# Kernel optimization log

Hardware: AMD Instinct MI355X
Metric: run time of the kernel (lower is better)

## Reference

```python
import jax, jax.numpy as jnp
import numpy as np
from jax import lax

HEADS = 8
DIM_HEAD = 64
LANDMARKS = 256
PINV_ITERS = 6
KERNEL = 33


def moore_penrose_iter_pinv(x, iters=PINV_ITERS):
    # x: [b, h, m, m]
    abs_x = jnp.abs(x)
    col = abs_x.sum(axis=-1)
    row = abs_x.sum(axis=-2)
    z = jnp.swapaxes(x, -1, -2) / (jnp.max(col) * jnp.max(row) + 1e-12)
    I = jnp.eye(x.shape[-1], dtype=x.dtype)  # broadcasts over b, h
    for _ in range(iters):
        xz = x @ z
        z = 0.25 * z @ (13.0 * I - xz @ (15.0 * I - xz @ (7.0 * I - xz)))
    return z


def setup_inputs() -> dict:
    key = jax.random.key(0)
    k1, k2, k3, k4, k5 = jax.random.split(key, 5)
    b, n, dim = 4, 8192, 512
    inner = HEADS * DIM_HEAD
    x = jax.random.normal(k1, (b, n, dim), dtype=jnp.float32)
    Wqkv = jax.random.normal(k2, (dim, inner * 3), dtype=jnp.float32) * (dim ** -0.5)
    Wout = jax.random.normal(k3, (inner, dim), dtype=jnp.float32) * (inner ** -0.5)
    bout = jax.random.normal(k4, (dim,), dtype=jnp.float32) * 0.02
    conv_w = jax.random.normal(k5, (HEADS, 1, KERNEL, 1), dtype=jnp.float32) * (KERNEL ** -0.5)
    return {"x": x, "Wqkv": Wqkv, "Wout": Wout, "bout": bout, "conv_w": conv_w}


def reference(x, Wqkv, Wout, bout, conv_w):
    b, n, dim = x.shape
    h, d, m = HEADS, DIM_HEAD, LANDMARKS
    scale = d ** -0.5
    # n is a multiple of m, so no left-padding branch; mask is None.
    qkv = x @ Wqkv  # [b, n, 3*h*d]
    q, k, v = jnp.split(qkv, 3, axis=-1)
    tohead = lambda t: t.reshape(b, n, h, d).transpose(0, 2, 1, 3)  # [b,h,n,d]
    q, k, v = tohead(q), tohead(k), tohead(v)
    q = q * scale
    l = n // m  # tokens per landmark group
    qL = q.reshape(b, h, m, l, d).sum(axis=3) / l  # [b,h,m,d]
    kL = k.reshape(b, h, m, l, d).sum(axis=3) / l
    attn1 = jax.nn.softmax(jnp.einsum('bhid,bhjd->bhij', q, kL), axis=-1)   # [b,h,n,m]
    attn2 = jax.nn.softmax(jnp.einsum('bhid,bhjd->bhij', qL, kL), axis=-1)  # [b,h,m,m]
    attn3 = jax.nn.softmax(jnp.einsum('bhid,bhjd->bhij', qL, k), axis=-1)   # [b,h,m,n]
    attn2_pinv = moore_penrose_iter_pinv(attn2, PINV_ITERS)
    out = attn1 @ (attn2_pinv @ (attn3 @ v))  # [b,h,n,d]
    # depthwise residual conv over v viewed as NCHW (C=heads, H=n, W=d)
    pad = KERNEL // 2
    res = lax.conv_general_dilated(
        v, conv_w, window_strides=(1, 1), padding=((pad, pad), (0, 0)),
        dimension_numbers=('NCHW', 'OIHW', 'NCHW'), feature_group_count=h)
    out = out + res
    out = out.transpose(0, 2, 1, 3).reshape(b, n, h * d)
    out = out @ Wout + bout
    return out
```

## Files before the change

### kernel.cpp

```cpp
#include <hip/hip_runtime.h>
#include <hip/hip_bf16.h>
#include <math.h>

#define BB 4
#define NH 8
#define NN 8192
#define DD 64
#define MM 256
#define LG 32
#define DIM 512
#define K3 1536
#define KER 33

typedef __hip_bfloat16 bf16;
typedef __attribute__((ext_vector_type(8))) short bf16x8;
typedef __attribute__((ext_vector_type(4))) float f32x4;

__device__ __forceinline__ float b2f(bf16 x) { return __bfloat162float(x); }
__device__ __forceinline__ bf16 f2b(float x) { return __float2bfloat16(x); }
__device__ __forceinline__ short f2bs(float x) { bf16 h = __float2bfloat16(x); return *reinterpret_cast<short*>(&h); }
__device__ __forceinline__ float bsf(short s) { return __uint_as_float(((unsigned int)(unsigned short)s) << 16); }
__device__ __forceinline__ float blo(unsigned int u) { return __uint_as_float(u << 16); }
__device__ __forceinline__ float bhi(unsigned int u) { return __uint_as_float(u & 0xffff0000u); }

__device__ __forceinline__ void g2lds16(const void* g, void* l) {
    __builtin_amdgcn_global_load_lds(
        (const __attribute__((address_space(1))) unsigned int*)g,
        (__attribute__((address_space(3))) unsigned int*)l, 16, 0, 0);
}

__global__ void zero_out(float* __restrict__ o) {
    o[(size_t)blockIdx.x * 256 + threadIdx.x] = 0.f;
}

__global__ void split_x(const float* __restrict__ x, short* __restrict__ xh,
                        short* __restrict__ xl) {
    size_t i = ((size_t)blockIdx.x * 256 + threadIdx.x) * 8;
    const float4* xp = (const float4*)(x + i);
    float4 v0 = xp[0], v1 = xp[1];
    float vv[8] = {v0.x, v0.y, v0.z, v0.w, v1.x, v1.y, v1.z, v1.w};
    short hb[8], lb[8];
#pragma unroll
    for (int u = 0; u < 8; u++) {
        bf16 h = f2b(vv[u]);
        hb[u] = *(short*)&h;
        lb[u] = f2bs(vv[u] - b2f(h));
    }
    *(uint4*)(xh + i) = *(uint4*)hb;
    *(uint4*)(xl + i) = *(uint4*)lb;
}

__global__ void split_wT(const float* __restrict__ W, short* __restrict__ wh,
                         short* __restrict__ wl, int Nn) {
    int idx = blockIdx.x * 256 + threadIdx.x;
    int k = idx & 511, n = idx >> 9;
    float v = W[(size_t)k * Nn + n];
    bf16 h = f2b(v);
    wh[idx] = *(short*)&h;
    wl[idx] = f2bs(v - b2f(h));
}

__global__ __launch_bounds__(256) void gemm_qkv_mfma(
        const short* __restrict__ xh, const short* __restrict__ xl,
        const short* __restrict__ wh, const short* __restrict__ wl,
        bf16* __restrict__ q, bf16* __restrict__ k, bf16* __restrict__ v) {
    __shared__ short Ah[128 * 32];
    __shared__ short Al[128 * 32];
    __shared__ short Bh[128 * 32];
    __shared__ short Bl[128 * 32];
    int orig = blockIdx.x;
    int wg = (orig & 7) * 384 + (orig >> 3);
    int by = wg / 12, bx = wg - by * 12;
    int rowBase = by * 128, colBase = bx * 128;
    int tid = threadIdx.x;
    int rl = tid >> 2;
    int ch = (tid & 3) * 8;
    int wave = tid >> 6, lane = tid & 63;
    int ln = lane & 15, quad = lane >> 4;
    int wr = (wave >> 1) * 64, wc = (wave & 1) * 64;
    f32x4 acc[4][4];
#pragma unroll
    for (int mt = 0; mt < 4; mt++)
#pragma unroll
        for (int nt = 0; nt < 4; nt++) acc[mt][nt] = (f32x4){0.f, 0.f, 0.f, 0.f};

    for (int k0 = 0; k0 < DIM; k0 += 32) {
        __syncthreads();
#pragma unroll
        for (int p = 0; p < 2; p++) {
            int r = p * 64 + rl;
            size_t ga = (size_t)(rowBase + r) * DIM + k0 + ch;
            size_t gb = (size_t)(colBase + r) * DIM + k0 + ch;
            int lo = r * 32 + ch;
            g2lds16(xh + ga, &Ah[lo]);
            g2lds16(xl + ga, &Al[lo]);
            g2lds16(wh + gb, &Bh[lo]);
            g2lds16(wl + gb, &Bl[lo]);
        }
        __syncthreads();
        bf16x8 a_h[4], a_l[4], b_h[4], b_l[4];
#pragma unroll
        for (int mt = 0; mt < 4; mt++) {
            int o = (wr + mt * 16 + ln) * 32 + quad * 8;
            a_h[mt] = *(const bf16x8*)&Ah[o];
            a_l[mt] = *(const bf16x8*)&Al[o];
        }
#pragma unroll
        for (int nt = 0; nt < 4; nt++) {
            int o = (wc + nt * 16 + ln) * 32 + quad * 8;
            b_h[nt] = *(const bf16x8*)&Bh[o];
            b_l[nt] = *(const bf16x8*)&Bl[o];
        }
#pragma unroll
        for (int mt = 0; mt < 4; mt++)
#pragma unroll
            for (int nt = 0; nt < 4; nt++) {
                acc[mt][nt] = __builtin_amdgcn_mfma_f32_16x16x32_bf16(a_h[mt], b_h[nt], acc[mt][nt], 0, 0, 0);
                acc[mt][nt] = __builtin_amdgcn_mfma_f32_16x16x32_bf16(a_l[mt], b_h[nt], acc[mt][nt], 0, 0, 0);
                acc[mt][nt] = __builtin_amdgcn_mfma_f32_16x16x32_bf16(a_h[mt], b_l[nt], acc[mt][nt], 0, 0, 0);
            }
    }
    int part = colBase >> 9;
    bf16* dst = part == 0 ? q : (part == 1 ? k : v);
    float scale = part == 0 ? 0.125f : 1.0f;
#pragma unroll
    for (int mt = 0; mt < 4; mt++)
#pragma unroll
        for (int nt = 0; nt < 4; nt++)
#pragma unroll
            for (int r = 0; r < 4; r++) {
                int row = rowBase + wr + mt * 16 + quad * 4 + r;
                int col = colBase + wc + nt * 16 + ln;
                int h = (col & 511) >> 6, d = col & 63;
                int b_ = row >> 13, n_ = row & 8191;
                size_t di = ((size_t)(b_ * NH + h) * NN + n_) * DD + d;
                dst[di] = f2b(acc[mt][nt][r] * scale);
            }
}

__global__ __launch_bounds__(256) void gemm_out_mfma(
        const bf16* __restrict__ A, const short* __restrict__ wh,
        const short* __restrict__ wl, const float* __restrict__ bias,
        float* __restrict__ C) {
    __shared__ short As[128 * 32];
    __shared__ short Bh[128 * 32];
    __shared__ short Bl[128 * 32];
    int orig = blockIdx.x;
    int wg = (orig & 7) * 128 + (orig >> 3);
    int by = wg >> 2, bx = wg & 3;
    int rowBase = by * 128, colBase = bx * 128;
    int tid = threadIdx.x;
    int rl = tid >> 2, ch = (tid & 3) * 8;
    int wave = tid >> 6, lane = tid & 63;
    int ln = lane & 15, quad = lane >> 4;
    int wr = (wave >> 1) * 64, wc = (wave & 1) * 64;
    const short* Ab = (const short*)A;
    f32x4 acc[4][4];
#pragma unroll
    for (int mt = 0; mt < 4; mt++)
#pragma unroll
        for (int nt = 0; nt < 4; nt++) acc[mt][nt] = (f32x4){0.f, 0.f, 0.f, 0.f};

    for (int k0 = 0; k0 < DIM; k0 += 32) {
        __syncthreads();
#pragma unroll
        for (int p = 0; p < 2; p++) {
            int r = p * 64 + rl;
            size_t ga = (size_t)(rowBase + r) * DIM + k0 + ch;
            size_t gb = (size_t)(colBase + r) * DIM + k0 + ch;
            int lo = r * 32 + ch;
            g2lds16(Ab + ga, &As[lo]);
            g2lds16(wh + gb, &Bh[lo]);
            g2lds16(wl + gb, &Bl[lo]);
        }
        __syncthreads();
        bf16x8 a[4], b_h[4], b_l[4];
#pragma unroll
        for (int mt = 0; mt < 4; mt++)
            a[mt] = *(const bf16x8*)&As[(wr + mt * 16 + ln) * 32 + quad * 8];
#pragma unroll
        for (int nt = 0; nt < 4; nt++) {
            int o = (wc + nt * 16 + ln) * 32 + quad * 8;
            b_h[nt] = *(const bf16x8*)&Bh[o];
            b_l[nt] = *(const bf16x8*)&Bl[o];
        }
#pragma unroll
        for (int mt = 0; mt < 4; mt++)
#pragma unroll
            for (int nt = 0; nt < 4; nt++) {
                acc[mt][nt] = __builtin_amdgcn_mfma_f32_16x16x32_bf16(a[mt], b_h[nt], acc[mt][nt], 0, 0, 0);
                acc[mt][nt] = __builtin_amdgcn_mfma_f32_16x16x32_bf16(a[mt], b_l[nt], acc[mt][nt], 0, 0, 0);
            }
    }
#pragma unroll
    for (int mt = 0; mt < 4; mt++)
#pragma unroll
        for (int nt = 0; nt < 4; nt++)
#pragma unroll
            for (int r = 0; r < 4; r++) {
                int row = rowBase + wr + mt * 16 + quad * 4 + r;
                int col = colBase + wc + nt * 16 + ln;
                C[(size_t)row * DIM + col] = acc[mt][nt][r] + bias[col];
            }
}

__global__ __launch_bounds__(256) void bgemm_pair(
        const short* __restrict__ Ah, const short* __restrict__ Al,
        const short* __restrict__ Bh, const short* __restrict__ Bl,
        short* __restrict__ oAh, short* __restrict__ oAl,
        short* __restrict__ oBh, short* __restrict__ oBl,
        float* __restrict__ oF, float scale, float alpha,
        float scaleB, float alphaB, int flags) {
    __shared__ short sAh[64 * 32];
    __shared__ short sAl[64 * 32];
    __shared__ short sBh[64 * 32];
    __shared__ short sBl[64 * 32];
    int bat = blockIdx.z;
    int rowBase = blockIdx.y * 64;
    int colBase = blockIdx.x * 64;
    const size_t MB = (size_t)bat * (MM * MM);
    int tid = threadIdx.x;
    int rl = tid >> 2, ch = (tid & 3) * 8;
    int wave = tid >> 6, lane = tid & 63;
    int ln = lane & 15, quad = lane >> 4;
    int wr = (wave >> 1) * 32, wc = (wave & 1) * 32;
    f32x4 acc[2][2];
#pragma unroll
    for (int mt = 0; mt < 2; mt++)
#pragma unroll
        for (int nt = 0; nt < 2; nt++) acc[mt][nt] = (f32x4){0.f, 0.f, 0.f, 0.f};

    for (int k0 = 0; k0 < MM; k0 += 32) {
        __syncthreads();
        {
            size_t ga = MB + (size_t)(rowBase + rl) * MM + k0 + ch;
            size_t gb = MB + (size_t)(colBase + rl) * MM + k0 + ch;
            int lo = rl * 32 + ch;
            g2lds16(Ah + ga, &sAh[lo]);
            g2lds16(Al + ga, &sAl[lo]);
            g2lds16(Bh + gb, &sBh[lo]);
            g2lds16(Bl + gb, &sBl[lo]);
        }
        __syncthreads();
        bf16x8 a_h[2], a_l[2], b_h[2], b_l[2];
#pragma unroll
        for (int mt = 0; mt < 2; mt++) {
            int o = (wr + mt * 16 + ln) * 32 + quad * 8;
            a_h[mt] = *(const bf16x8*)&sAh[o];
            a_l[mt] = *(const bf16x8*)&sAl[o];
        }
#pragma unroll
        for (int nt = 0; nt < 2; nt++) {
            int o = (wc + nt * 16 + ln) * 32 + quad * 8;
            b_h[nt] = *(const bf16x8*)&sBh[o];
            b_l[nt] = *(const bf16x8*)&sBl[o];
        }
#pragma unroll
        for (int mt = 0; mt < 2; mt++)
#pragma unroll
            for (int nt = 0; nt < 2; nt++) {
                acc[mt][nt] = __builtin_amdgcn_mfma_f32_16x16x32_bf16(a_h[mt], b_h[nt], acc[mt][nt], 0, 0, 0);
                acc[mt][nt] = __builtin_amdgcn_mfma_f32_16x16x32_bf16(a_l[mt], b_h[nt], acc[mt][nt], 0, 0, 0);
                acc[mt][nt] = __builtin_amdgcn_mfma_f32_16x16x32_bf16(a_h[mt], b_l[nt], acc[mt][nt], 0, 0, 0);
            }
    }
#pragma unroll
    for (int mt = 0; mt < 2; mt++)
#pragma unroll
        for (int nt = 0; nt < 2; nt++) {
            short bh4[4], bl4[4];
            int col = colBase + wc + nt * 16 + ln;
            int row0 = rowBase + wr + mt * 16 + quad * 4;
#pragma unroll
            for (int r = 0; r < 4; r++) {
                int row = row0 + r;
                float val = scale * acc[mt][nt][r];
                if (row == col) val += alpha;
                if (flags & 4) oF[MB + (size_t)row * MM + col] = val;
                if (flags & 1) {
                    short vh = f2bs(val);
                    oAh[MB + (size_t)row * MM + col] = vh;
                    oAl[MB + (size_t)row * MM + col] = f2bs(val - bsf(vh));
                }
                float bv = scaleB * val;
                if (row == col) bv += alphaB;
                short bvh = f2bs(bv);
                bh4[r] = bvh; bl4[r] = f2bs(bv - bsf(bvh));
            }
            if (flags & 2) {
                size_t o = MB + (size_t)col * MM + row0;
                *(uint2*)&oBh[o] = *(uint2*)bh4;
                *(uint2*)&oBl[o] = *(uint2*)bl4;
            }
        }
}

__global__ void z_init_split(const float* __restrict__ x2, const float* __restrict__ scal,
                             short* __restrict__ x2Ah, short* __restrict__ x2Al,
                             short* __restrict__ zAh, short* __restrict__ zAl,
                             short* __restrict__ zBh, short* __restrict__ zBl) {
    size_t base = ((size_t)blockIdx.x * 256 + threadIdx.x) * 8;
    float inv = 1.0f / (scal[0] + 1e-12f);
    int c0 = (int)(base & 255);
    int r = (int)((base >> 8) & 255);
    size_t MB = (base >> 16) << 16;
    const float4* xp = (const float4*)(x2 + base);
    float4 v0 = xp[0], v1 = xp[1];
    float vv[8] = {v0.x, v0.y, v0.z, v0.w, v1.x, v1.y, v1.z, v1.w};
    short ho[8], lo_[8], h2[8], l2[8];
#pragma unroll
    for (int u = 0; u < 8; u++) {
        short xh = f2bs(vv[u]);
        h2[u] = xh; l2[u] = f2bs(vv[u] - bsf(xh));
        float zv = vv[u] * inv;
        short zh = f2bs(zv);
        ho[u] = zh; lo_[u] = f2bs(zv - bsf(zh));
    }
    *(uint4*)&x2Ah[base] = *(uint4*)h2;
    *(uint4*)&x2Al[base] = *(uint4*)l2;
    *(uint4*)&zBh[base] = *(uint4*)ho;
    *(uint4*)&zBl[base] = *(uint4*)lo_;
#pragma unroll
    for (int u = 0; u < 8; u++) {
        float v = x2[MB + (size_t)(c0 + u) * MM + r] * inv;
        short vh = f2bs(v);
        ho[u] = vh; lo_[u] = f2bs(v - bsf(vh));
    }
    *(uint4*)&zAh[base] = *(uint4*)ho;
    *(uint4*)&zAl[base] = *(uint4*)lo_;
}

__global__ void bgemm_t2t(const float* __restrict__ A, const float* __restrict__ B,
                          short* __restrict__ T) {
    __shared__ float As[16][64];
    __shared__ float Bs[16][64];
    int bat = blockIdx.z;
    const float* Ab = A + (size_t)bat * MM * MM;
    const float* Bb = B + (size_t)bat * MM * DD;
    short* Tb = T + (size_t)bat * DD * MM;
    int tid = threadIdx.x;
    int rowBase = blockIdx.y * 64;
    int ty = tid >> 4, tx = tid & 15;
    float acc[4][4] = {};
    for (int k0 = 0; k0 < MM; k0 += 16) {
        for (int idx = tid; idx < 64 * 16; idx += 256) {
            int r = idx >> 4, c = idx & 15;
            As[c][r] = Ab[(size_t)(rowBase + r) * MM + k0 + c];
        }
        for (int idx = tid; idx < 16 * 64; idx += 256) {
            int r = idx >> 6, c = idx & 63;
            Bs[r][c] = Bb[(size_t)(k0 + r) * DD + c];
        }
        __syncthreads();
#pragma unroll
        for (int kk = 0; kk < 16; kk++) {
            float a[4], b[4];
#pragma unroll
            for (int i = 0; i < 4; i++) a[i] = As[kk][ty * 4 + i];
#pragma unroll
            for (int j = 0; j < 4; j++) b[j] = Bs[kk][tx * 4 + j];
#pragma unroll
            for (int i = 0; i < 4; i++)
#pragma unroll
                for (int j = 0; j < 4; j++) acc[i][j] += a[i] * b[j];
        }
        __syncthreads();
    }
#pragma unroll
    for (int i = 0; i < 4; i++) {
        int r = rowBase + ty * 4 + i;
#pragma unroll
        for (int j = 0; j < 4; j++) {
            int c = tx * 4 + j;
            Tb[(size_t)c * MM + r] = f2bs(acc[i][j]);
        }
    }
}

__global__ void landmark_means(const bf16* __restrict__ q, const bf16* __restrict__ k,
                               float* __restrict__ qL, float* __restrict__ kL) {
    int idx = blockIdx.x * 256 + threadIdx.x;
    int d = idx & 63;
    int mi = (idx >> 6) & 255;
    int bh = idx >> 14;
    const bf16* qp = q + ((size_t)bh * NN + mi * LG) * DD + d;
    const bf16* kp = k + ((size_t)bh * NN + mi * LG) * DD + d;
    float sq = 0.f, sk = 0.f;
#pragma unroll
    for (int j = 0; j < LG; j++) { sq += b2f(qp[(size_t)j * DD]); sk += b2f(kp[(size_t)j * DD]); }
    qL[idx] = sq * (1.f / LG);
    kL[idx] = sk * (1.f / LG);
}

__global__ void kl_to_bf16(const float* __restrict__ kL, short* __restrict__ kl16) {
    size_t i = ((size_t)blockIdx.x * 256 + threadIdx.x) * 4;
    float4 v = *(const float4*)(kL + i);
    short o[4] = {f2bs(v.x), f2bs(v.y), f2bs(v.z), f2bs(v.w)};
    *(uint2*)&kl16[i] = *(uint2*)o;
}

__global__ void attn2_softmax(const float* __restrict__ qL, const float* __restrict__ kL,
                              float* __restrict__ x2) {
    __shared__ float qs[64];
    __shared__ float red[256];
    int bh = blockIdx.x >> 8, i = blockIdx.x & 255;
    int t = threadIdx.x;
    if (t < 64) qs[t] = qL[((size_t)bh * MM + i) * DD + t];
    __syncthreads();
    const float4* kp = (const float4*)(kL + ((size_t)bh * MM + t) * DD);
    float l = 0.f;
#pragma unroll
    for (int u = 0; u < 16; u++) {
        float4 kv = kp[u];
        l += qs[u*4+0]*kv.x + qs[u*4+1]*kv.y + qs[u*4+2]*kv.z + qs[u*4+3]*kv.w;
    }
    red[t] = l; __syncthreads();
    for (int s = 128; s > 0; s >>= 1) { if (t < s) red[t] = fmaxf(red[t], red[t + s]); __syncthreads(); }
    float mx = red[0]; __syncthreads();
    float e = __expf(l - mx);
    red[t] = e; __syncthreads();
    for (int s = 128; s > 0; s >>= 1) { if (t < s) red[t] += red[t + s]; __syncthreads(); }
    x2[((size_t)bh * MM + i) * MM + t] = e / red[0];
}

__global__ void init_scal(float* scal) {
    if (threadIdx.x == 0) { scal[0] = 0.f; scal[1] = 0.f; }
}

__global__ void csum_max(const float* __restrict__ x2, float* scal) {
    __shared__ float red[256];
    int t = threadIdx.x;
    const float* xp = x2 + (size_t)blockIdx.x * MM * MM;
    float s = 0.f;
    for (int i = 0; i < MM; i++) s += fabsf(xp[(size_t)i * MM + t]);
    red[t] = s; __syncthreads();
    for (int st = 128; st > 0; st >>= 1) { if (t < st) red[t] = fmaxf(red[t], red[t + st]); __syncthreads(); }
    if (t == 0) atomicMax((unsigned int*)&scal[0], __float_as_uint(red[0]));
}

__global__ void transpose_v(const bf16* __restrict__ v, bf16* __restrict__ vT) {
    int gw = blockIdx.x * 4 + (threadIdx.x >> 6);
    int lane = threadIdx.x & 63;
    int bh = gw >> 8;
    int c  = gw & 255;
    const bf16* vb = v + ((size_t)bh * NN + c * 32) * DD + lane;
    unsigned short buf[32];
#pragma unroll
    for (int i = 0; i < 32; i++) buf[i] = *(const unsigned short*)(vb + (size_t)i * DD);
    bf16* dst = vT + ((size_t)bh * DD + lane) * NN + c * 32;
#pragma unroll
    for (int u = 0; u < 4; u++)
        *(uint4*)(dst + u * 8) = *(uint4*)&buf[u * 8];
}

#define NJ 128
#define KS2 72
#define VS2 136
#define PS2 136
__global__ __launch_bounds__(128, 2) void attn3v_mfma(
        const float* __restrict__ qL, const bf16* __restrict__ k,
        const bf16* __restrict__ vT, float* __restrict__ t1) {
    __shared__ short ks[NJ * KS2];
    __shared__ short vs[DD * VS2];
    __shared__ short ps[2][16 * PS2];
    int g = blockIdx.x;
    int c = g & 7, t = g >> 3;
    int bh = c + 8 * (t >> 3);
    int r0 = (t & 7) * 32;
    int tid = threadIdx.x;
    int wave = tid >> 6, lane = tid & 63;
    int ln = lane & 15, quad = lane >> 4;
    int m = r0 + wave * 16 + ln;
    const float* qrow = qL + ((size_t)bh * MM + m) * DD;
    bf16x8 a0, a1;
#pragma unroll
    for (int u = 0; u < 8; u++) {
        ((short*)&a0)[u] = f2bs(qrow[quad * 8 + u]);
        ((short*)&a1)[u] = f2bs(qrow[32 + quad * 8 + u]);
    }
    const uint4* kg = (const uint4*)(k + (size_t)bh * NN * DD);
    const uint4* vg = (const uint4*)(vT + (size_t)bh * DD * NN);
    float mrow[4], lrow[4];
    f32x4 o[4];
#pragma unroll
    for (int r = 0; r < 4; r++) { mrow[r] = -1e30f; lrow[r] = 0.f; }
#pragma unroll
    for (int ct = 0; ct < 4; ct++) o[ct] = (f32x4){0.f, 0.f, 0.f, 0.f};
    short* pw = &ps[wave][0];

    for (int j0 = 0; j0 < NN; j0 += NJ) {
        __syncthreads();
#pragma unroll
        for (int it = 0; it < 8; it++) {
            int idx = it * 128 + tid;
            int row = idx >> 3, c8 = idx & 7;
            uint4 pk = kg[(size_t)(j0 + row) * 8 + c8];
            *(uint4*)&ks[row * KS2 + c8 * 8] = pk;
        }
#pragma unroll
        for (int it = 0; it < 8; it++) {
            int idx = it * 128 + tid;
            int row = idx >> 4, c8 = idx & 15;
            uint4 pv = vg[(size_t)row * (NN / 8) + (j0 / 8) + c8];
            *(uint4*)&vs[row * VS2 + c8 * 8] = pv;
        }
        __syncthreads();
        f32x4 s[8];
#pragma unroll
        for (int ct = 0; ct < 8; ct++) {
            const short* kp = &ks[(ct * 16 + ln) * KS2 + quad * 8];
            bf16x8 b0 = *(const bf16x8*)kp;
            bf16x8 b1 = *(const bf16x8*)(kp + 32);
            f32x4 cc = {0.f, 0.f, 0.f, 0.f};
            cc = __builtin_amdgcn_mfma_f32_16x16x32_bf16(a0, b0, cc, 0, 0, 0);
            cc = __builtin_amdgcn_mfma_f32_16x16x32_bf16(a1, b1, cc, 0, 0, 0);
            s[ct] = cc;
        }
#pragma unroll
        for (int r = 0; r < 4; r++) {
            float v = -1e30f;
#pragma unroll
            for (int ct = 0; ct < 8; ct++) v = fmaxf(v, s[ct][r]);
            v = fmaxf(v, __shfl_xor(v, 1));
            v = fmaxf(v, __shfl_xor(v, 2));
            v = fmaxf(v, __shfl_xor(v, 4));
            v = fmaxf(v, __shfl_xor(v, 8));
            float mn = fmaxf(mrow[r], v);
            float alpha = __expf(mrow[r] - mn);
            mrow[r] = mn;
            float psum = 0.f;
#pragma unroll
            for (int ct = 0; ct < 8; ct++) { float e = __expf(s[ct][r] - mn); s[ct][r] = e; psum += e; }
            lrow[r] = lrow[r] * alpha + psum;
#pragma unroll
            for (int c2 = 0; c2 < 4; c2++) o[c2][r] *= alpha;
        }
#pragma unroll
        for (int ct = 0; ct < 8; ct++)
#pragma unroll
            for (int r = 0; r < 4; r++)
                pw[(quad * 4 + r) * PS2 + ct * 16 + ln] = f2bs(s[ct][r]);
#pragma unroll
        for (int kstep = 0; kstep < 4; kstep++) {
            bf16x8 pa = *(const bf16x8*)&pw[ln * PS2 + kstep * 32 + quad * 8];
#pragma unroll
            for (int ct = 0; ct < 4; ct++) {
                bf16x8 pb = *(const bf16x8*)&vs[(ct * 16 + ln) * VS2 + kstep * 32 + quad * 8];
                o[ct] = __builtin_amdgcn_mfma_f32_16x16x32_bf16(pa, pb, o[ct], 0, 0, 0);
            }
        }
    }
#pragma unroll
    for (int r = 0; r < 4; r++) {
        float l = lrow[r];
        l += __shfl_xor(l, 1);
        l += __shfl_xor(l, 2);
        l += __shfl_xor(l, 4);
        l += __shfl_xor(l, 8);
        lrow[r] = 1.0f / l;
    }
#pragma unroll
    for (int ct = 0; ct < 4; ct++)
#pragma unroll
        for (int r = 0; r < 4; r++) {
            int row = r0 + wave * 16 + quad * 4 + r;
            t1[((size_t)bh * MM + row) * DD + ct * 16 + ln] = o[ct][r] * lrow[r];
        }
}

#define T2S 264
#define VLS 72
__global__ __launch_bounds__(256, 3) void attn1_mfma(
        const bf16* __restrict__ q, const short* __restrict__ kl16,
        const short* __restrict__ t2t, const bf16* __restrict__ v,
        const float* __restrict__ cw, bf16* __restrict__ oh) {
    __shared__ short ps1[4][16 * T2S];
    __shared__ short vload[96 * VLS];
    int bh = blockIdx.y;
    int n0 = blockIdx.x * 64;
    int tid = threadIdx.x;
    int b_ = bh >> 3, h = bh & 7;
    const bf16* vb = v + (size_t)bh * NN * DD;
    for (int idx = tid; idx < 96 * 8; idx += 256) {
        int row = idx >> 3, c8 = (idx & 7) * 8;
        int gn = n0 - 16 + row;
        uint4 pv;
        pv.x = pv.y = pv.z = pv.w = 0u;
        if (gn >= 0 && gn < NN) pv = *(const uint4*)(vb + (size_t)gn * DD + c8);
        *(uint4*)&vload[row * VLS + c8] = pv;
    }
    int wave = tid >> 6, lane = tid & 63;
    int ln = lane & 15, quad = lane >> 4;
    int m = n0 + wave * 16 + ln;
    const bf16* qrow = q + ((size_t)bh * NN + m) * DD;
    bf16x8 a0 = *(const bf16x8*)(qrow + quad * 8);
    bf16x8 a1 = *(const bf16x8*)(qrow + 32 + quad * 8);
    const short* klb = kl16 + (size_t)bh * MM * DD;
    f32x4 acc[16];
#pragma unroll
    for (int nt = 0; nt < 16; nt++) {
        const short* kp = klb + (nt * 16 + ln) * DD + quad * 8;
        bf16x8 b0 = *(const bf16x8*)kp;
        bf16x8 b1 = *(const bf16x8*)(kp + 32);
        f32x4 c = {0.f, 0.f, 0.f, 0.f};
        c = __builtin_amdgcn_mfma_f32_16x16x32_bf16(a0, b0, c, 0, 0, 0);
        c = __builtin_amdgcn_mfma_f32_16x16x32_bf16(a1, b1, c, 0, 0, 0);
        acc[nt] = c;
    }
    float inv[4];
#pragma unroll
    for (int r = 0; r < 4; r++) {
        float vx = -1e30f;
#pragma unroll
        for (int nt = 0; nt < 16; nt++) vx = fmaxf(vx, acc[nt][r]);
        vx = fmaxf(vx, __shfl_xor(vx, 1));
        vx = fmaxf(vx, __shfl_xor(vx, 2));
        vx = fmaxf(vx, __shfl_xor(vx, 4));
        vx = fmaxf(vx, __shfl_xor(vx, 8));
        float s = 0.f;
#pragma unroll
        for (int nt = 0; nt < 16; nt++) { float e = __expf(acc[nt][r] - vx); acc[nt][r] = e; s += e; }
        s += __shfl_xor(s, 1);
        s += __shfl_xor(s, 2);
        s += __shfl_xor(s, 4);
        s += __shfl_xor(s, 8);
        inv[r] = 1.0f / s;
    }
    short* pw = &ps1[wave][0];
#pragma unroll
    for (int nt = 0; nt < 16; nt++)
#pragma unroll
        for (int r = 0; r < 4; r++)
            pw[(quad * 4 + r) * T2S + nt * 16 + ln] = f2bs(acc[nt][r]);
    __syncthreads();
    const short* t2b = t2t + (size_t)bh * DD * MM;
    f32x4 o[4];
#pragma unroll
    for (int nt = 0; nt < 4; nt++) o[nt] = (f32x4){0.f, 0.f, 0.f, 0.f};
#pragma unroll
    for (int ks = 0; ks < 8; ks++) {
        bf16x8 pa = *(const bf16x8*)&pw[ln * T2S + ks * 32 + quad * 8];
#pragma unroll
        for (int nt = 0; nt < 4; nt++) {
            bf16x8 pb = *(const bf16x8*)(t2b + (nt * 16 + ln) * MM + ks * 32 + quad * 8);
            o[nt] = __builtin_amdgcn_mfma_f32_16x16x32_bf16(pa, pb, o[nt], 0, 0, 0);
        }
    }
    const float* wrow = cw + h * KER;
    int lbase = wave * 16 + quad * 4;
#pragma unroll
    for (int nt = 0; nt < 4; nt++) {
        int d = nt * 16 + ln;
        float win[36];
#pragma unroll
        for (int j = 0; j < 36; j++)
            win[j] = bsf(vload[(lbase + j) * VLS + d]);
        float res[4] = {0.f, 0.f, 0.f, 0.f};
#pragma unroll
        for (int t = 0; t < KER; t++) {
            float wt = wrow[t];
#pragma unroll
            for (int r = 0; r < 4; r++) res[r] += wt * win[r + t];
        }
#pragma unroll
        for (int r = 0; r < 4; r++) {
            int row = n0 + lbase + r;
            oh[((size_t)(b_ * NN + row)) * DIM + h * 64 + d] = f2b(o[nt][r] * inv[r] + res[r]);
        }
    }
}


extern "C" void kernel_launch(void* const* d_in, const int* in_sizes, int n_in,
                              void* d_out, int out_size, void* d_ws, size_t ws_size,
                              hipStream_t stream) {
    const float* x    = (const float*)d_in[0];
    const float* Wqkv = (const float*)d_in[1];
    const float* Wout = (const float*)d_in[2];
    const float* bout = (const float*)d_in[3];
    const float* cw   = (const float*)d_in[4];
    float* out = (float*)d_out;

    const size_t SZ_QKV = (size_t)BB * NH * NN * DD;
    const size_t SZ_L   = (size_t)BB * NH * MM * DD;
    const size_t SZ_M2  = (size_t)BB * NH * MM * MM;

    char* p = (char*)d_ws;
    bf16* q    = (bf16*)p;  p += SZ_QKV * 2;
    bf16* v    = (bf16*)p;  p += SZ_QKV * 2;
    float* x2   = (float*)p; p += SZ_M2 * 4;
    float* zf   = (float*)p; p += SZ_M2 * 4;
    float* z2r  = (float*)p; p += SZ_M2 * 4;
    float* bAr  = (float*)p; p += SZ_M2 * 4;
    float* bBr  = (float*)p; p += SZ_M2 * 4;
    float* qL   = (float*)p; p += SZ_L * 4;
    float* kL   = (float*)p; p += SZ_L * 4;
    float* t1   = (float*)p; p += SZ_L * 4;
    short* t2t  = (short*)p; p += SZ_L * 4;
    float* scal = (float*)p; p += 2 * 4;
    size_t need = (size_t)(p - (char*)d_ws);
    bf16* k  = (bf16*)d_out;
    bf16* vT = (bf16*)d_out + SZ_QKV;
    bf16* oh = (bf16*)x2;

    short* xh  = (short*)x2;
    short* xl  = (short*)vT;
    short* wqh = (short*)bBr;
    short* wql = (short*)bBr + (size_t)K3 * DIM;
    short* woh = (short*)q;
    short* wol = (short*)q + (size_t)DIM * DIM;
    short* kl16 = (short*)t1;

    const size_t U = SZ_M2;
    short* db = (short*)d_out;
    short* bufBTh = db + 0 * U;  short* bufBTl = db + 1 * U;
    short* z2BTh  = db + 2 * U;  short* z2BTl  = db + 3 * U;
    short* zPair[2][4] = {
        { db + 4 * U, db + 5 * U, db + 6 * U, db + 7 * U },
        { db + 8 * U, db + 9 * U, db + 10 * U, db + 11 * U } };
    short* x2Ah = (short*)z2r;   short* x2Al = (short*)z2r + U;
    short* bufAh = (short*)bAr;  short* bufAl = (short*)bAr + U;

    if (ws_size < need) {
        zero_out<<<out_size / 256, 256, 0, stream>>>(out);
        return;
    }

    split_x<<<(int)(SZ_QKV / (256 * 8)), 256, 0, stream>>>(x, xh, xl);
    split_wT<<<(K3 * DIM) / 256, 256, 0, stream>>>(Wqkv, wqh, wql, K3);
    gemm_qkv_mfma<<<3072, 256, 0, stream>>>(xh, xl, wqh, wql, q, k, v);
    transpose_v<<<(BB * NH * MM) / 4, 256, 0, stream>>>(v, vT);
    landmark_means<<<(BB * NH * MM * DD) / 256, 256, 0, stream>>>(q, k, qL, kL);
    attn2_softmax<<<BB * NH * MM, 256, 0, stream>>>(qL, kL, x2);
    attn3v_mfma<<<256, 128, 0, stream>>>(qL, k, vT, t1);
    init_scal<<<1, 64, 0, stream>>>(scal);
    csum_max<<<BB * NH, 256, 0, stream>>>(x2, scal);
    z_init_split<<<(int)(SZ_M2 / (256 * 8)), 256, 0, stream>>>(
        x2, scal, x2Ah, x2Al,
        zPair[0][0], zPair[0][1], zPair[0][2], zPair[0][3]);
    int cur = 0;
    for (int it = 0; it < 6; it++) {
        int nxt = cur ^ 1;
        bgemm_pair<<<dim3(4, 4, BB * NH), 256, 0, stream>>>(
            x2Ah, x2Al, zPair[cur][2], zPair[cur][3],
            bufAh, bufAl, bufBTh, bufBTl, nullptr,
            1.f, 0.f, -1.f, 7.f, 1 | 2);
        bgemm_pair<<<dim3(4, 4, BB * NH), 256, 0, stream>>>(
            bufAh, bufAl, bufBTh, bufBTl,
            nullptr, nullptr, z2BTh, z2BTl, nullptr,
            -1.f, 15.f, 1.f, 0.f, 2);
        bgemm_pair<<<dim3(4, 4, BB * NH), 256, 0, stream>>>(
            bufAh, bufAl, z2BTh, z2BTl,
            nullptr, nullptr, bufBTh, bufBTl, nullptr,
            -1.f, 13.f, 1.f, 0.f, 2);
        int fl = (it == 5) ? 4 : (1 | 2);
        bgemm_pair<<<dim3(4, 4, BB * NH), 256, 0, stream>>>(
            zPair[cur][0], zPair[cur][1], bufBTh, bufBTl,
            zPair[nxt][0], zPair[nxt][1], zPair[nxt][2], zPair[nxt][3],
            zf, 0.25f, 0.f, 1.f, 0.f, fl);
        cur = nxt;
    }
    bgemm_t2t<<<dim3(1, 4, BB * NH), 256, 0, stream>>>(zf, t1, t2t);
    kl_to_bf16<<<(int)(SZ_L / (256 * 4)), 256, 0, stream>>>(kL, kl16);
    attn1_mfma<<<dim3(NN / 64, BB * NH), 256, 0, stream>>>(q, kl16, t2t, v, cw, oh);
    split_wT<<<(DIM * DIM) / 256, 256, 0, stream>>>(Wout, woh, wol, DIM);
    gemm_out_mfma<<<1024, 256, 0, stream>>>(oh, woh, wol, bout, out);

    (void)in_sizes; (void)n_in; (void)ws_size;
}
```

Baseline: 1.044 ms.

## Split attn3v key range across wave pairs and transpose conv window in LDS

The attn3v kernel now runs 256 threads per block. Two wave pairs each process alternating 128-key chunks with their own K/V shared buffers, and their online-softmax states (max, sum, output) are merged through shared memory at the end. This doubles parallelism over the sequential 8192-key loop, since only 256 blocks were launched, at the cost of more LDS and a merge step. Separately, attn1 stores the v window transposed in LDS so each lane reads its 36-tap conv window with 8-byte vector loads instead of strided scalar reads.

```diff
diff --git a/kernel.cpp b/kernel.cpp
--- a/kernel.cpp
+++ b/kernel.cpp
@@ -457,20 +457,23 @@
 #define KS2 72
 #define VS2 136
 #define PS2 136
-__global__ __launch_bounds__(128, 2) void attn3v_mfma(
+__global__ __launch_bounds__(256) void attn3v_mfma(
         const float* __restrict__ qL, const bf16* __restrict__ k,
         const bf16* __restrict__ vT, float* __restrict__ t1) {
-    __shared__ short ks[NJ * KS2];
-    __shared__ short vs[DD * VS2];
-    __shared__ short ps[2][16 * PS2];
+    __shared__ short ks[2][NJ * KS2];
+    __shared__ short vs[2][DD * VS2];
+    __shared__ short ps[4][16 * PS2];
+    __shared__ float mb[128 * 25];
     int g = blockIdx.x;
     int c = g & 7, t = g >> 3;
     int bh = c + 8 * (t >> 3);
     int r0 = (t & 7) * 32;
     int tid = threadIdx.x;
     int wave = tid >> 6, lane = tid & 63;
+    int pair = wave >> 1, wv = wave & 1;
+    int ptid = tid & 127;
     int ln = lane & 15, quad = lane >> 4;
-    int m = r0 + wave * 16 + ln;
+    int m = r0 + wv * 16 + ln;
     const float* qrow = qL + ((size_t)bh * MM + m) * DD;
     bf16x8 a0, a1;
 #pragma unroll
@@ -487,28 +490,31 @@
 #pragma unroll
     for (int ct = 0; ct < 4; ct++) o[ct] = (f32x4){0.f, 0.f, 0.f, 0.f};
     short* pw = &ps[wave][0];
-
-    for (int j0 = 0; j0 < NN; j0 += NJ) {
-        __syncthreads();
-#pragma unroll
-        for (int it = 0; it < 8; it++) {
-            int idx = it * 128 + tid;
+    short* ksp = &ks[pair][0];
+    short* vsp = &vs[pair][0];
+
+    for (int it = 0; it < NN / (2 * NJ); it++) {
+        int j0 = (2 * it + pair) * NJ;
+        __syncthreads();
+#pragma unroll
+        for (int s = 0; s < 8; s++) {
+            int idx = s * 128 + ptid;
             int row = idx >> 3, c8 = idx & 7;
             uint4 pk = kg[(size_t)(j0 + row) * 8 + c8];
-            *(uint4*)&ks[row * KS2 + c8 * 8] = pk;
-        }
-#pragma unroll
-        for (int it = 0; it < 8; it++) {
-            int idx = it * 128 + tid;
+            *(uint4*)&ksp[row * KS2 + c8 * 8] = pk;
+        }
+#pragma unroll
+        for (int s = 0; s < 8; s++) {
+            int idx = s * 128 + ptid;
             int row = idx >> 4, c8 = idx & 15;
             uint4 pv = vg[(size_t)row * (NN / 8) + (j0 / 8) + c8];
-            *(uint4*)&vs[row * VS2 + c8 * 8] = pv;
+            *(uint4*)&vsp[row * VS2 + c8 * 8] = pv;
         }
         __syncthreads();
         f32x4 s[8];
 #pragma unroll
         for (int ct = 0; ct < 8; ct++) {
-            const short* kp = &ks[(ct * 16 + ln) * KS2 + quad * 8];
+            const short* kp = &ksp[(ct * 16 + ln) * KS2 + quad * 8];
             bf16x8 b0 = *(const bf16x8*)kp;
             bf16x8 b1 = *(const bf16x8*)(kp + 32);
             f32x4 cc = {0.f, 0.f, 0.f, 0.f};
@@ -545,37 +551,62 @@
             bf16x8 pa = *(const bf16x8*)&pw[ln * PS2 + kstep * 32 + quad * 8];
 #pragma unroll
             for (int ct = 0; ct < 4; ct++) {
-                bf16x8 pb = *(const bf16x8*)&vs[(ct * 16 + ln) * VS2 + kstep * 32 + quad * 8];
+                bf16x8 pb = *(const bf16x8*)&vsp[(ct * 16 + ln) * VS2 + kstep * 32 + quad * 8];
                 o[ct] = __builtin_amdgcn_mfma_f32_16x16x32_bf16(pa, pb, o[ct], 0, 0, 0);
             }
         }
     }
-#pragma unroll
-    for (int r = 0; r < 4; r++) {
-        float l = lrow[r];
-        l += __shfl_xor(l, 1);
-        l += __shfl_xor(l, 2);
-        l += __shfl_xor(l, 4);
-        l += __shfl_xor(l, 8);
-        lrow[r] = 1.0f / l;
-    }
-#pragma unroll
-    for (int ct = 0; ct < 4; ct++)
+    __syncthreads();
+    if (wave >= 2) {
+        float* mp = &mb[(tid - 128) * 25];
+#pragma unroll
+        for (int r = 0; r < 4; r++) { mp[r] = mrow[r]; mp[4 + r] = lrow[r]; }
+#pragma unroll
+        for (int ct = 0; ct < 4; ct++)
+#pragma unroll
+            for (int r = 0; r < 4; r++) mp[8 + ct * 4 + r] = o[ct][r];
+    }
+    __syncthreads();
+    if (wave < 2) {
+        const float* mp = &mb[(wave * 64 + lane) * 25];
 #pragma unroll
         for (int r = 0; r < 4; r++) {
-            int row = r0 + wave * 16 + quad * 4 + r;
-            t1[((size_t)bh * MM + row) * DD + ct * 16 + ln] = o[ct][r] * lrow[r];
-        }
+            float mB = mp[r], lB = mp[4 + r];
+            float mn = fmaxf(mrow[r], mB);
+            float eA = __expf(mrow[r] - mn);
+            float eB = __expf(mB - mn);
+            lrow[r] = lrow[r] * eA + lB * eB;
+#pragma unroll
+            for (int ct = 0; ct < 4; ct++)
+                o[ct][r] = o[ct][r] * eA + mp[8 + ct * 4 + r] * eB;
+        }
+#pragma unroll
+        for (int r = 0; r < 4; r++) {
+            float l = lrow[r];
+            l += __shfl_xor(l, 1);
+            l += __shfl_xor(l, 2);
+            l += __shfl_xor(l, 4);
+            l += __shfl_xor(l, 8);
+            lrow[r] = 1.0f / l;
+        }
+#pragma unroll
+        for (int ct = 0; ct < 4; ct++)
+#pragma unroll
+            for (int r = 0; r < 4; r++) {
+                int row = r0 + wv * 16 + quad * 4 + r;
+                t1[((size_t)bh * MM + row) * DD + ct * 16 + ln] = o[ct][r] * lrow[r];
+            }
+    }
 }
 
 #define T2S 264
-#define VLS 72
+#define VTS 108
 __global__ __launch_bounds__(256, 3) void attn1_mfma(
         const bf16* __restrict__ q, const short* __restrict__ kl16,
         const short* __restrict__ t2t, const bf16* __restrict__ v,
         const float* __restrict__ cw, bf16* __restrict__ oh) {
     __shared__ short ps1[4][16 * T2S];
-    __shared__ short vload[96 * VLS];
+    __shared__ short vt[64 * VTS];
     int bh = blockIdx.y;
     int n0 = blockIdx.x * 64;
     int tid = threadIdx.x;
@@ -587,7 +618,10 @@
         uint4 pv;
         pv.x = pv.y = pv.z = pv.w = 0u;
         if (gn >= 0 && gn < NN) pv = *(const uint4*)(vb + (size_t)gn * DD + c8);
-        *(uint4*)&vload[row * VLS + c8] = pv;
+        short tmp[8];
+        *(uint4*)tmp = pv;
+#pragma unroll
+        for (int u = 0; u < 8; u++) vt[(c8 + u) * VTS + row] = tmp[u];
     }
     int wave = tid >> 6, lane = tid & 63;
     int ln = lane & 15, quad = lane >> 4;
@@ -651,10 +685,14 @@
 #pragma unroll
     for (int nt = 0; nt < 4; nt++) {
         int d = nt * 16 + ln;
+        const short* vrow = &vt[d * VTS + lbase];
         float win[36];
 #pragma unroll
-        for (int j = 0; j < 36; j++)
-            win[j] = bsf(vload[(lbase + j) * VLS + d]);
+        for (int j4 = 0; j4 < 9; j4++) {
+            uint2 w4 = *(const uint2*)(vrow + j4 * 4);
+            win[j4 * 4 + 0] = blo(w4.x); win[j4 * 4 + 1] = bhi(w4.x);
+            win[j4 * 4 + 2] = blo(w4.y); win[j4 * 4 + 3] = bhi(w4.y);
+        }
         float res[4] = {0.f, 0.f, 0.f, 0.f};
 #pragma unroll
         for (int t = 0; t < KER; t++) {
@@ -732,7 +770,7 @@
     transpose_v<<<(BB * NH * MM) / 4, 256, 0, stream>>>(v, vT);
     landmark_means<<<(BB * NH * MM * DD) / 256, 256, 0, stream>>>(q, k, qL, kL);
     attn2_softmax<<<BB * NH * MM, 256, 0, stream>>>(qL, kL, x2);
-    attn3v_mfma<<<256, 128, 0, stream>>>(qL, k, vT, t1);
+    attn3v_mfma<<<256, 256, 0, stream>>>(qL, k, vT, t1);
     init_scal<<<1, 64, 0, stream>>>(scal);
     csum_max<<<BB * NH, 256, 0, stream>>>(x2, scal);
     z_init_split<<<(int)(SZ_M2 / (256 * 8)), 256, 0, stream>>>(
```

Measured after the change: 1.005 ms. 3.7% less time.
